# Kernel optimization log

Hardware: AMD Instinct MI355X
Metric: run time of the kernel (lower is better)

## Reference

```python
import jax, jax.numpy as jnp
import numpy as np

NUM_GROUPS = 2048  # ix values drawn from [0, NUM_GROUPS); stands in for torch.unique's group count

def setup_inputs() -> dict:
    key = jax.random.key(0)
    ks = jax.random.split(key, 9)
    B, E, D = 2, 32768, 512
    s = 1.0 / np.sqrt(D)  # nn.Linear default init scale
    x = jax.random.normal(ks[0], (B, E, D), jnp.float32)
    ix = jax.random.randint(ks[1], (E,), 0, NUM_GROUPS)
    Wf = jax.random.uniform(ks[2], (D, D), jnp.float32, -s, s)
    bf = jax.random.uniform(ks[3], (D,), jnp.float32, -s, s)
    Wg = jax.random.uniform(ks[4], (D, D), jnp.float32, -s, s)
    bg = jax.random.uniform(ks[5], (D,), jnp.float32, -s, s)
    Wh = jax.random.uniform(ks[6], (D, D), jnp.float32, -s, s)
    bh = jax.random.uniform(ks[7], (D,), jnp.float32, -s, s)
    return {"x": x, "ix": ix, "Wf": Wf, "bf": bf, "Wg": Wg, "bg": bg, "Wh": Wh, "bh": bh}

def reference(x, ix, Wf, bf, Wg, bg, Wh, bh):
    # Linear projections (nn.Linear: x @ W.T + b)
    logits = jnp.einsum('bed,kd->bek', x, Wg) + bg  # g(x): (B,E,D)
    vals   = jnp.einsum('bed,kd->bek', x, Wf) + bf  # f(x): (B,E,D)
    # Move edges to leading axis for segment ops: (E,B,D)
    lt = jnp.transpose(logits, (1, 0, 2))
    vt = jnp.transpose(vals, (1, 0, 2))
    # Group-wise (scatter) softmax over edges sharing the same ix
    m = jax.ops.segment_max(lt, ix, num_segments=NUM_GROUPS)      # (G,B,D)
    e = jnp.exp(lt - m[ix])                                        # (E,B,D)
    denom = jax.ops.segment_sum(e, ix, num_segments=NUM_GROUPS)   # (G,B,D)
    w = e / denom[ix]                                              # (E,B,D)
    # Weighted scatter-sum per group
    y = jax.ops.segment_sum(vt * w, ix, num_segments=NUM_GROUPS)  # (G,B,D)
    y = jnp.transpose(y, (1, 0, 2))                                # (B,G,D)
    out = jnp.einsum('bgd,kd->bgk', y, Wh) + bh                    # h(y)
    return out[:, ix]                                              # expand back to (B,E,D)
```

## Files before the change

### kernel.cpp

```cpp
#include <hip/hip_runtime.h>
#include <hip/hip_bf16.h>
#include <cstdint>
#include <cstddef>

typedef __bf16 bf16x8 __attribute__((ext_vector_type(8)));
typedef float f32x4 __attribute__((ext_vector_type(4)));
using u16 = unsigned short;

#define NUM_GROUPS_C 2048

__device__ __forceinline__ u16 f2bf(float f) {
  union { float f; uint32_t u; } c; c.f = f;
  uint32_t r = (c.u + 0x7fffu + ((c.u >> 16) & 1u)) >> 16;
  return (u16)r;
}
__device__ __forceinline__ float bf2f(u16 h) {
  union { uint32_t u; float f; } c; c.u = ((uint32_t)h) << 16; return c.f;
}

__global__ void cast_f32_bf16(const float* __restrict__ src, u16* __restrict__ dst, long n4) {
  long i = (long)blockIdx.x * blockDim.x + threadIdx.x;
  long stride = (long)gridDim.x * blockDim.x;
  for (; i < n4; i += stride) {
    float4 v = reinterpret_cast<const float4*>(src)[i];
    uint2 o;
    o.x = (uint32_t)f2bf(v.x) | ((uint32_t)f2bf(v.y) << 16);
    o.y = (uint32_t)f2bf(v.z) | ((uint32_t)f2bf(v.w) << 16);
    reinterpret_cast<uint2*>(dst)[i] = o;
  }
}

__global__ void zero_i32(int* p, int n) {
  int i = blockIdx.x * blockDim.x + threadIdx.x;
  if (i < n) p[i] = 0;
}
__global__ void count_k(const int* __restrict__ ix, int* __restrict__ cnt, int E) {
  int e = blockIdx.x * blockDim.x + threadIdx.x;
  if (e < E) atomicAdd(&cnt[ix[e]], 1);
}
__global__ void scan_k(const int* __restrict__ cnt, int* __restrict__ offs,
                       int* __restrict__ cursor, int G) {
  __shared__ int part[256];
  int t = threadIdx.x;
  int gpt = G / 256;
  int base = t * gpt;
  int loc[8];
  int s = 0;
  for (int j = 0; j < gpt; ++j) { loc[j] = cnt[base + j]; s += loc[j]; }
  part[t] = s;
  __syncthreads();
  for (int off = 1; off < 256; off <<= 1) {
    int v = (t >= off) ? part[t - off] : 0;
    __syncthreads();
    part[t] += v;
    __syncthreads();
  }
  int run = part[t] - s;
  for (int j = 0; j < gpt; ++j) {
    offs[base + j] = run;
    cursor[base + j] = run;
    run += loc[j];
  }
}
__global__ void scatter_k(const int* __restrict__ ix, int* __restrict__ cursor,
                          int* __restrict__ elist, int E) {
  int e = blockIdx.x * blockDim.x + threadIdx.x;
  if (e < E) {
    int g = ix[e];
    int pos = atomicAdd(&cursor[g], 1);
    elist[pos] = e;
  }
}

__device__ __forceinline__ void stage_tile_128x64(const u16* __restrict__ src, int ld,
                                                  u16* lds, int tid) {
  int wid = tid >> 6;
  #pragma unroll
  for (int i = 0; i < 4; ++i) {
    int c = i * 256 + tid;
    const u16* g = src + (size_t)(c >> 3) * ld + ((c & 7) << 3);
    char* l = (char*)lds + ((i * 4 + wid) << 10);
    __builtin_amdgcn_global_load_lds((const __attribute__((address_space(1))) void*)g,
                                     (__attribute__((address_space(3))) void*)l, 16, 0, 0);
  }
}

template <typename OT>
__device__ __forceinline__ void store_c(OT* C, size_t idx, float v);
template <>
__device__ __forceinline__ void store_c<u16>(u16* C, size_t idx, float v) { C[idx] = f2bf(v); }
template <>
__device__ __forceinline__ void store_c<float>(float* C, size_t idx, float v) { C[idx] = v; }

template <typename OT>
__global__ __launch_bounds__(256)
void gemm_bf16_nt(const u16* __restrict__ A,
                  const u16* __restrict__ B0, const u16* __restrict__ B1,
                  const float* __restrict__ bias0, const float* __restrict__ bias1,
                  OT* __restrict__ C0, OT* __restrict__ C1,
                  int K, int N, int ntilesPerMat) {
  __shared__ u16 sA[128 * 64];
  __shared__ u16 sB[128 * 64];

  int tid = threadIdx.x;
  int mt = blockIdx.x;
  int nt = blockIdx.y;
  const u16* Bm = B0; const float* bias = bias0; OT* C = C0;
  if (nt >= ntilesPerMat) { Bm = B1; bias = bias1; C = C1; nt -= ntilesPerMat; }

  const int m0 = mt * 128, n0 = nt * 128;
  const u16* Ap = A + (size_t)m0 * K;
  const u16* Bp = Bm + (size_t)n0 * K;

  int lane = tid & 63;
  int wid = tid >> 6;
  int wm = wid >> 1, wn = wid & 1;
  int fr = lane & 15;
  int fq = lane >> 4;

  f32x4 acc[4][4] = {};

  for (int k0 = 0; k0 < K; k0 += 64) {
    stage_tile_128x64(Ap + k0, K, sA, tid);
    stage_tile_128x64(Bp + k0, K, sB, tid);
    __syncthreads();
    #pragma unroll
    for (int kk = 0; kk < 2; ++kk) {
      bf16x8 af[4], bfrag[4];
      #pragma unroll
      for (int mi = 0; mi < 4; ++mi)
        af[mi] = *reinterpret_cast<const bf16x8*>(&sA[(wm * 64 + mi * 16 + fr) * 64 + kk * 32 + fq * 8]);
      #pragma unroll
      for (int nj = 0; nj < 4; ++nj)
        bfrag[nj] = *reinterpret_cast<const bf16x8*>(&sB[(wn * 64 + nj * 16 + fr) * 64 + kk * 32 + fq * 8]);
      #pragma unroll
      for (int mi = 0; mi < 4; ++mi)
        #pragma unroll
        for (int nj = 0; nj < 4; ++nj)
          acc[mi][nj] = __builtin_amdgcn_mfma_f32_16x16x32_bf16(af[mi], bfrag[nj], acc[mi][nj], 0, 0, 0);
    }
    __syncthreads();
  }

  #pragma unroll
  for (int nj = 0; nj < 4; ++nj) {
    int col = n0 + wn * 64 + nj * 16 + fr;
    float bv = bias[col];
    #pragma unroll
    for (int mi = 0; mi < 4; ++mi) {
      int rowb = m0 + wm * 64 + mi * 16 + fq * 4;
      #pragma unroll
      for (int r = 0; r < 4; ++r) {
        store_c<OT>(C, (size_t)(rowb + r) * N + col, acc[mi][nj][r] + bv);
      }
    }
  }
}

__global__ __launch_bounds__(256)
void seg_softmax(const u16* __restrict__ lg, const u16* __restrict__ vl,
                 const int* __restrict__ cnt, const int* __restrict__ offs,
                 const int* __restrict__ elist,
                 u16* __restrict__ y, int E, int D, int B, int G) {
  __shared__ int eids[256];
  int g = blockIdx.x / B;
  int b = blockIdx.x - g * B;
  int t = threadIdx.x;
  int n = cnt[g], start = offs[g];
  int d0 = t * 2;

  float m0 = -1e30f, m1 = -1e30f, s0 = 0.f, s1 = 0.f, a0 = 0.f, a1 = 0.f;
  for (int c0 = 0; c0 < n; c0 += 256) {
    int nc = n - c0; if (nc > 256) nc = 256;
    __syncthreads();
    if (t < nc) eids[t] = elist[start + c0 + t];
    __syncthreads();
    for (int i = 0; i < nc; ++i) {
      size_t base = ((size_t)b * E + eids[i]) * D + d0;
      uint32_t lu = *reinterpret_cast<const uint32_t*>(lg + base);
      uint32_t vu = *reinterpret_cast<const uint32_t*>(vl + base);
      float l0 = bf2f((u16)(lu & 0xffffu)), l1 = bf2f((u16)(lu >> 16));
      float v0 = bf2f((u16)(vu & 0xffffu)), v1 = bf2f((u16)(vu >> 16));
      float nm0 = fmaxf(m0, l0);
      float sc0 = __expf(m0 - nm0), w0 = __expf(l0 - nm0);
      s0 = s0 * sc0 + w0; a0 = a0 * sc0 + w0 * v0; m0 = nm0;
      float nm1 = fmaxf(m1, l1);
      float sc1 = __expf(m1 - nm1), w1 = __expf(l1 - nm1);
      s1 = s1 * sc1 + w1; a1 = a1 * sc1 + w1 * v1; m1 = nm1;
    }
  }
  float r0 = (n > 0) ? a0 / s0 : 0.f;
  float r1 = (n > 0) ? a1 / s1 : 0.f;
  size_t yoff = ((size_t)b * G + g) * D + d0;
  uint32_t o = (uint32_t)f2bf(r0) | ((uint32_t)f2bf(r1) << 16);
  *reinterpret_cast<uint32_t*>(y + yoff) = o;
}

__global__ void gather_k(const float* __restrict__ of, const int* __restrict__ ix,
                         float* __restrict__ out, int E, int D, int G) {
  int be = blockIdx.x;
  int b = be / E;
  int e = be - b * E;
  int gsel = ix[e];
  const float4* src = reinterpret_cast<const float4*>(of + ((size_t)b * G + gsel) * D);
  float4* dst = reinterpret_cast<float4*>(out + (size_t)be * D);
  for (int t = threadIdx.x; t < D / 4; t += blockDim.x)
    dst[t] = src[t];
}

extern "C" void kernel_launch(void* const* d_in, const int* in_sizes, int n_in,
                              void* d_out, int out_size, void* d_ws, size_t ws_size,
                              hipStream_t stream) {
  const float* x   = (const float*)d_in[0];
  const int*   ix  = (const int*)d_in[1];
  const float* Wf  = (const float*)d_in[2];
  const float* bfb = (const float*)d_in[3];
  const float* Wg  = (const float*)d_in[4];
  const float* bg  = (const float*)d_in[5];
  const float* Wh  = (const float*)d_in[6];
  const float* bh  = (const float*)d_in[7];

  const int E = in_sizes[1];
  const int D = in_sizes[3];
  const int B = in_sizes[0] / (E * D);
  const int G = NUM_GROUPS_C;
  const int M = B * E;
  const long xn = (long)M * D;

  char* ws = (char*)d_ws;
  size_t off = 0;
  auto alloc = [&](size_t bytes) -> char* {
    char* p = ws + off;
    off += (bytes + 255) & ~(size_t)255;
    return p;
  };
  u16* xb  = (u16*)alloc((size_t)M * D * 2);
  u16* lgb = (u16*)alloc((size_t)M * D * 2);
  u16* vlb = (u16*)alloc((size_t)M * D * 2);
  u16* Wgb = (u16*)alloc((size_t)D * D * 2);
  u16* Wfb = (u16*)alloc((size_t)D * D * 2);
  u16* Whb = (u16*)alloc((size_t)D * D * 2);
  u16* yb  = (u16*)alloc((size_t)B * G * D * 2);
  float* ofb = (float*)alloc((size_t)B * G * D * 4);
  int* cnt    = (int*)alloc((size_t)G * 4);
  int* offs   = (int*)alloc((size_t)G * 4);
  int* cursor = (int*)alloc((size_t)G * 4);
  int* elist  = (int*)alloc((size_t)E * 4);

  cast_f32_bf16<<<2048, 256, 0, stream>>>(x, xb, xn / 4);
  cast_f32_bf16<<<64, 256, 0, stream>>>(Wg, Wgb, (long)D * D / 4);
  cast_f32_bf16<<<64, 256, 0, stream>>>(Wf, Wfb, (long)D * D / 4);
  cast_f32_bf16<<<64, 256, 0, stream>>>(Wh, Whb, (long)D * D / 4);

  zero_i32<<<(G + 255) / 256, 256, 0, stream>>>(cnt, G);
  count_k<<<(E + 255) / 256, 256, 0, stream>>>(ix, cnt, E);
  scan_k<<<1, 256, 0, stream>>>(cnt, offs, cursor, G);
  scatter_k<<<(E + 255) / 256, 256, 0, stream>>>(ix, cursor, elist, E);

  dim3 gfg(M / 128, 2 * (D / 128));
  gemm_bf16_nt<u16><<<gfg, 256, 0, stream>>>(xb, Wgb, Wfb, bg, bfb, lgb, vlb, D, D, D / 128);

  seg_softmax<<<G * B, 256, 0, stream>>>(lgb, vlb, cnt, offs, elist, yb, E, D, B, G);

  dim3 gh((B * G) / 128, D / 128);
  gemm_bf16_nt<float><<<gh, 256, 0, stream>>>(yb, Whb, Whb, bh, bh, ofb, ofb, D, D, D / 128);

  gather_k<<<B * E, 128, 0, stream>>>(ofb, ix, (float*)d_out, E, D, G);
}
```

Measured before the change: 262.1 us.

## Replace projection GEMM with 256x256 double-buffered swizzled-LDS kernel

The fused logits/values projection GEMM now runs as a new 512-thread kernel with 256x256 output tiles, double-buffered async global-to-LDS staging, an XOR-swizzled LDS layout that avoids bank conflicts, and workgroup index swizzling for L2 locality. It is meant to raise MFMA utilisation and data reuse over the old 128x128 single-buffered kernel. The output GEMM keeps the old kernel, specialised to f32 output. The larger tile needs 128KB of LDS and many accumulator registers, and the large M dimension leaves fewer workgroups in flight.

```diff
diff --git a/kernel.cpp b/kernel.cpp
--- a/kernel.cpp
+++ b/kernel.cpp
@@ -16,6 +16,11 @@
 }
 __device__ __forceinline__ float bf2f(u16 h) {
   union { uint32_t u; float f; } c; c.u = ((uint32_t)h) << 16; return c.f;
+}
+
+__device__ __forceinline__ void glds16(const u16* g, void* l) {
+  __builtin_amdgcn_global_load_lds((const __attribute__((address_space(1))) void*)g,
+                                   (__attribute__((address_space(3))) void*)l, 16, 0, 0);
 }
 
 __global__ void cast_f32_bf16(const float* __restrict__ src, u16* __restrict__ dst, long n4) {
@@ -72,6 +77,115 @@
   }
 }
 
+__global__ __launch_bounds__(512, 2)
+void gemm256_bf16_nt(const u16* __restrict__ A,
+                     const u16* __restrict__ B0, const u16* __restrict__ B1,
+                     const float* __restrict__ bias0, const float* __restrict__ bias1,
+                     u16* __restrict__ C0, u16* __restrict__ C1,
+                     int K, int N) {
+  __shared__ u16 lds[2 * 32768];
+
+  const int tid  = threadIdx.x;
+  const int lane = tid & 63;
+  const int wid  = tid >> 6;
+  const int wm   = wid >> 2;
+  const int wn   = wid & 3;
+  const int fr   = lane & 15;
+  const int fq   = lane >> 4;
+  const int swr  = fr & 7;
+
+  const int nwg = gridDim.x;
+  const int cpx = nwg >> 3;
+  const int wg  = blockIdx.x;
+  const int swz = (wg & 7) * cpx + (wg >> 3);
+  const int mt = swz >> 2;
+  const int ns = swz & 3;
+  const u16* Bm  = (ns < 2) ? B0 : B1;
+  const float* bias = (ns < 2) ? bias0 : bias1;
+  u16* C = (ns < 2) ? C0 : C1;
+  const int n0 = (ns & 1) * 256;
+  const int m0 = mt * 256;
+
+  const int r8   = tid >> 3;
+  const int scol = ((tid & 7) ^ (r8 & 7)) << 3;
+  const u16* Ab = A  + (size_t)m0 * K + scol;
+  const u16* Bb = Bm + (size_t)n0 * K + scol;
+
+  auto stage = [&](int buf, int k0) {
+    u16* bufA = lds + buf * 32768;
+    u16* bufB = bufA + 16384;
+    #pragma unroll
+    for (int i = 0; i < 4; ++i)
+      glds16(Ab + (size_t)(i * 64 + r8) * K + k0, (char*)bufA + i * 8192 + wid * 1024);
+    #pragma unroll
+    for (int i = 0; i < 4; ++i)
+      glds16(Bb + (size_t)(i * 64 + r8) * K + k0, (char*)bufB + i * 8192 + wid * 1024);
+  };
+
+  f32x4 acc[8][4] = {};
+  const int NT = K >> 6;
+
+  stage(0, 0);
+
+  for (int t = 0; t < NT; ++t) {
+    const int c = t & 1;
+    if (t + 1 < NT) {
+      stage(c ^ 1, (t + 1) << 6);
+      asm volatile("s_waitcnt vmcnt(8)" ::: "memory");
+    } else {
+      asm volatile("s_waitcnt vmcnt(0)" ::: "memory");
+    }
+    __builtin_amdgcn_s_barrier();
+
+    const char* sA_ = (const char*)(lds + c * 32768);
+    const char* sB_ = sA_ + 32768;
+
+    #pragma unroll
+    for (int q = 0; q < 4; ++q) {
+      const int qm = q >> 1, qn = q & 1;
+      bf16x8 av[4][2], bv[2][2];
+      #pragma unroll
+      for (int j = 0; j < 4; ++j)
+        #pragma unroll
+        for (int kk = 0; kk < 2; ++kk)
+          av[j][kk] = *(const bf16x8*)(sA_ + ((wm * 128 + (qm * 4 + j) * 16 + fr) << 7)
+                                           + ((((kk << 2) | fq) ^ swr) << 4));
+      #pragma unroll
+      for (int j = 0; j < 2; ++j)
+        #pragma unroll
+        for (int kk = 0; kk < 2; ++kk)
+          bv[j][kk] = *(const bf16x8*)(sB_ + ((wn * 64 + (qn * 2 + j) * 16 + fr) << 7)
+                                           + ((((kk << 2) | fq) ^ swr) << 4));
+      __builtin_amdgcn_s_barrier();
+      __builtin_amdgcn_s_setprio(1);
+      #pragma unroll
+      for (int j = 0; j < 4; ++j)
+        #pragma unroll
+        for (int jn = 0; jn < 2; ++jn)
+          #pragma unroll
+          for (int kk = 0; kk < 2; ++kk)
+            acc[qm * 4 + j][qn * 2 + jn] = __builtin_amdgcn_mfma_f32_16x16x32_bf16(
+                av[j][kk], bv[jn][kk], acc[qm * 4 + j][qn * 2 + jn], 0, 0, 0);
+      __builtin_amdgcn_s_setprio(0);
+      __builtin_amdgcn_s_barrier();
+      __builtin_amdgcn_sched_barrier(0);
+    }
+  }
+
+  #pragma unroll
+  for (int mi = 0; mi < 8; ++mi) {
+    const int row = m0 + wm * 128 + mi * 16 + fq * 4;
+    #pragma unroll
+    for (int ni = 0; ni < 4; ++ni) {
+      const int col = n0 + wn * 64 + ni * 16 + fr;
+      const float bvv = bias[col];
+      #pragma unroll
+      for (int r = 0; r < 4; ++r)
+        C[(size_t)(row + r) * N + col] = f2bf(acc[mi][ni][r] + bvv);
+    }
+  }
+}
+
 __device__ __forceinline__ void stage_tile_128x64(const u16* __restrict__ src, int ld,
                                                   u16* lds, int tid) {
   int wid = tid >> 6;
@@ -80,35 +194,19 @@
     int c = i * 256 + tid;
     const u16* g = src + (size_t)(c >> 3) * ld + ((c & 7) << 3);
     char* l = (char*)lds + ((i * 4 + wid) << 10);
-    __builtin_amdgcn_global_load_lds((const __attribute__((address_space(1))) void*)g,
-                                     (__attribute__((address_space(3))) void*)l, 16, 0, 0);
-  }
-}
-
-template <typename OT>
-__device__ __forceinline__ void store_c(OT* C, size_t idx, float v);
-template <>
-__device__ __forceinline__ void store_c<u16>(u16* C, size_t idx, float v) { C[idx] = f2bf(v); }
-template <>
-__device__ __forceinline__ void store_c<float>(float* C, size_t idx, float v) { C[idx] = v; }
-
-template <typename OT>
+    glds16(g, l);
+  }
+}
+
 __global__ __launch_bounds__(256)
-void gemm_bf16_nt(const u16* __restrict__ A,
-                  const u16* __restrict__ B0, const u16* __restrict__ B1,
-                  const float* __restrict__ bias0, const float* __restrict__ bias1,
-                  OT* __restrict__ C0, OT* __restrict__ C1,
-                  int K, int N, int ntilesPerMat) {
+void gemm_bf16_nt_f32out(const u16* __restrict__ A, const u16* __restrict__ Bm,
+                         const float* __restrict__ bias,
+                         float* __restrict__ C, int K, int N) {
   __shared__ u16 sA[128 * 64];
   __shared__ u16 sB[128 * 64];
 
   int tid = threadIdx.x;
-  int mt = blockIdx.x;
-  int nt = blockIdx.y;
-  const u16* Bm = B0; const float* bias = bias0; OT* C = C0;
-  if (nt >= ntilesPerMat) { Bm = B1; bias = bias1; C = C1; nt -= ntilesPerMat; }
-
-  const int m0 = mt * 128, n0 = nt * 128;
+  const int m0 = blockIdx.x * 128, n0 = blockIdx.y * 128;
   const u16* Ap = A + (size_t)m0 * K;
   const u16* Bp = Bm + (size_t)n0 * K;
 
@@ -150,9 +248,8 @@
     for (int mi = 0; mi < 4; ++mi) {
       int rowb = m0 + wm * 64 + mi * 16 + fq * 4;
       #pragma unroll
-      for (int r = 0; r < 4; ++r) {
-        store_c<OT>(C, (size_t)(rowb + r) * N + col, acc[mi][nj][r] + bv);
-      }
+      for (int r = 0; r < 4; ++r)
+        C[(size_t)(rowb + r) * N + col] = acc[mi][nj][r] + bv;
     }
   }
 }
@@ -257,13 +354,12 @@
   scan_k<<<1, 256, 0, stream>>>(cnt, offs, cursor, G);
   scatter_k<<<(E + 255) / 256, 256, 0, stream>>>(ix, cursor, elist, E);
 
-  dim3 gfg(M / 128, 2 * (D / 128));
-  gemm_bf16_nt<u16><<<gfg, 256, 0, stream>>>(xb, Wgb, Wfb, bg, bfb, lgb, vlb, D, D, D / 128);
+  gemm256_bf16_nt<<<(M / 256) * 4, 512, 0, stream>>>(xb, Wgb, Wfb, bg, bfb, lgb, vlb, D, D);
 
   seg_softmax<<<G * B, 256, 0, stream>>>(lgb, vlb, cnt, offs, elist, yb, E, D, B, G);
 
   dim3 gh((B * G) / 128, D / 128);
-  gemm_bf16_nt<float><<<gh, 256, 0, stream>>>(yb, Whb, Whb, bh, bh, ofb, ofb, D, D, D / 128);
+  gemm_bf16_nt_f32out<<<gh, 256, 0, stream>>>(yb, Whb, bh, ofb, D, D);
 
   gather_k<<<B * E, 128, 0, stream>>>(ofb, ix, (float*)d_out, E, D, G);
 }
```

Measured after the change: 242.2 us. 7.6% less time.
